# Kernel tuning notes

Measured on AMD Instinct MI355X. Metric: run time of the kernel, lower is better.

## Reference

```python
import jax, jax.numpy as jnp
import numpy as np

N, T, D, H, E, ED = 4096, 16, 5, 128, 32768, 32

def _leaky(x):
    return jnp.where(x >= 0, x, 0.2 * x)

def _lstm(x, Wih, Whh, bih, bhh):
    # x: [N, T, D] -> hidden sequence [N, T, H]; PyTorch gate order i,f,g,o
    pre = jnp.einsum('ntd,gd->tng', x, Wih) + bih + bhh  # [T, N, 4H]
    Hd = Whh.shape[1]
    def step(carry, p):
        h, c = carry
        g = p + h @ Whh.T
        i, f, gg, o = jnp.split(g, 4, axis=-1)
        c = jax.nn.sigmoid(f) * c + jax.nn.sigmoid(i) * jnp.tanh(gg)
        h = jax.nn.sigmoid(o) * jnp.tanh(c)
        return (h, c), h
    z = jnp.zeros((x.shape[0], Hd), x.dtype)
    _, hs = jax.lax.scan(step, (z, z), pre)
    return jnp.swapaxes(hs, 0, 1)

def _sire(x, src, dst, efeat, Wq, bq, Wk, bk, We, be, Wr, br):
    # SIREConv with agg_type='sum': m = LeakyReLU(eq[dst]+ek[src]+e); sum over in-edges; then linear_relation
    eq = x @ Wq.T + bq            # [N, T, H]
    ek = x @ Wk.T + bk            # [N, T, H]
    e = efeat @ We.T + be         # [E, H]
    m = _leaky(eq[dst] + ek[src] + e[:, None, :])  # [E, T, H]
    ft = jax.ops.segment_sum(m, dst, num_segments=x.shape[0])  # [N, T, H]
    return ft @ Wr.T + br

def _forward(stock_features, srcs, dsts, efeats, sire_ps, lstm_p, attn_p, mlp_p):
    sf = stock_features / jnp.mean(stock_features, axis=1, keepdims=True)
    sr = _lstm(sf, *lstm_p)  # [N, T, H]
    outs = [sr]
    for s, d, ef, p in zip(srcs, dsts, efeats, sire_ps):
        outs.append(_sire(sr, s, d, ef, *p))
    cat = jnp.concatenate(outs, axis=-1)  # [N, T, 4H]
    aw = jax.nn.softmax(cat @ attn_p[0].T + attn_p[1], axis=-2)  # softmax over time
    pooled = jnp.sum(cat * aw, axis=-2)   # [N, 4H]
    W1, b1, W2, b2 = mlp_p
    h = _leaky(pooled @ W1.T + b1)
    out = _leaky(h @ W2.T + b2)           # [N, 1]
    return out / sf[:, -1, 0:1] - 1.0


def setup_inputs() -> dict:
    key = jax.random.key(0)
    ks = iter(jax.random.split(key, 64))
    def nrm(shape, s=0.05):
        return jax.random.normal(next(ks), shape, jnp.float32) * s
    inp = {}
    inp['stock_features'] = jax.random.uniform(next(ks), (N, T, D), jnp.float32) + 0.5
    for g in ['wiki', 'industry', 'corr']:
        inp[g + '_src'] = jax.random.randint(next(ks), (E,), 0, N, jnp.int32)
        inp[g + '_dst'] = jax.random.randint(next(ks), (E,), 0, N, jnp.int32)
        inp[g + '_efeat'] = nrm((E, ED), 1.0)
        inp[g + '_Wq'] = nrm((H, H)); inp[g + '_bq'] = nrm((H,))
        inp[g + '_Wk'] = nrm((H, H)); inp[g + '_bk'] = nrm((H,))
        inp[g + '_We'] = nrm((H, ED)); inp[g + '_be'] = nrm((H,))
        inp[g + '_Wr'] = nrm((H, H)); inp[g + '_br'] = nrm((H,))
    inp['lstm_Wih'] = nrm((4 * H, D)); inp['lstm_Whh'] = nrm((4 * H, H))
    inp['lstm_bih'] = nrm((4 * H,)); inp['lstm_bhh'] = nrm((4 * H,))
    inp['attn_W'] = nrm((1, 4 * H)); inp['attn_b'] = nrm((1,))
    inp['mlp_W1'] = nrm((H, 4 * H)); inp['mlp_b1'] = nrm((H,))
    inp['mlp_W2'] = nrm((1, H)); inp['mlp_b2'] = nrm((1,))
    return inp


def reference(stock_features, wiki_src, wiki_dst, wiki_efeat,
              wiki_Wq, wiki_bq, wiki_Wk, wiki_bk, wiki_We, wiki_be, wiki_Wr, wiki_br,
              industry_src, industry_dst, industry_efeat,
              industry_Wq, industry_bq, industry_Wk, industry_bk, industry_We, industry_be, industry_Wr, industry_br,
              corr_src, corr_dst, corr_efeat,
              corr_Wq, corr_bq, corr_Wk, corr_bk, corr_We, corr_be, corr_Wr, corr_br,
              lstm_Wih, lstm_Whh, lstm_bih, lstm_bhh,
              attn_W, attn_b, mlp_W1, mlp_b1, mlp_W2, mlp_b2):
    srcs = (wiki_src, industry_src, corr_src)
    dsts = (wiki_dst, industry_dst, corr_dst)
    efeats = (wiki_efeat, industry_efeat, corr_efeat)
    sire_ps = ((wiki_Wq, wiki_bq, wiki_Wk, wiki_bk, wiki_We, wiki_be, wiki_Wr, wiki_br),
               (industry_Wq, industry_bq, industry_Wk, industry_bk, industry_We, industry_be, industry_Wr, industry_br),
               (corr_Wq, corr_bq, corr_Wk, corr_bk, corr_We, corr_be, corr_Wr, corr_br))
    return _forward(stock_features, srcs, dsts, efeats, sire_ps,
                    (lstm_Wih, lstm_Whh, lstm_bih, lstm_bhh),
                    (attn_W, attn_b), (mlp_W1, mlp_b1, mlp_W2, mlp_b2))
```

## Files before the change

### kernel.cpp

```cpp
#include <hip/hip_runtime.h>
#include <cstdint>
#include <cstddef>

#define NS 4096
#define TS 16
#define DF 5
#define HD 128
#define EE 32768
#define EDD 32

typedef __attribute__((ext_vector_type(8))) short bf16x8;
typedef __attribute__((ext_vector_type(4))) float f32x4;

__device__ __forceinline__ float sigmoidf_(float x){ return 1.f/(1.f+__expf(-x)); }
__device__ __forceinline__ float tanhf_(float x){ return 1.f - 2.f/(1.f+__expf(2.f*x)); }
__device__ __forceinline__ float leaky_(float x){ return x >= 0.f ? x : 0.2f*x; }

__device__ __forceinline__ unsigned short f2bf(float x){
  unsigned u = __float_as_uint(x);
  u += 0x7FFF + ((u>>16)&1);
  return (unsigned short)(u>>16);
}
__device__ __forceinline__ unsigned packbf(float a, float b){
  return (unsigned)f2bf(a) | ((unsigned)f2bf(b)<<16);
}
__device__ __forceinline__ void unpack2(unsigned u, float& a, float& b){
  a = __uint_as_float(u<<16);
  b = __uint_as_float(u & 0xFFFF0000u);
}
__device__ __forceinline__ void unpack8(uint4 q, float* f){
  unpack2(q.x, f[0], f[1]); unpack2(q.y, f[2], f[3]);
  unpack2(q.z, f[4], f[5]); unpack2(q.w, f[6], f[7]);
}
__device__ __forceinline__ bf16x8 ld_bf8(const unsigned short* p){
  union { uint4 u; bf16x8 v; } x; x.u = *(const uint4*)p; return x.v;
}

template<int ABF, int CBF>
__device__ __forceinline__ void gemm_dev(const void* Av, int lda,
    const float* __restrict__ Bp, int ldb, const float* __restrict__ bp,
    void* Cv, int ldc, int K, int act, size_t m0,
    unsigned short* Asb, unsigned short* Bsb)
{
  int tid = threadIdx.x;
  int wv = tid>>6, lane = tid&63, lm = lane&15, lq = lane>>4;
  f32x4 acc[2][8];
  #pragma unroll
  for (int mt=0;mt<2;mt++)
    #pragma unroll
    for (int nt=0;nt<8;nt++)
      acc[mt][nt] = (f32x4){0.f,0.f,0.f,0.f};

  for (int k0=0; k0<K; k0+=32){
    if (ABF){
      const unsigned short* A = (const unsigned short*)Av;
      #pragma unroll
      for (int rep=0;rep<2;rep++){
        int idx = tid + rep*256;
        int row = idx>>2, c8 = idx&3;
        *(uint4*)&Asb[row*40 + c8*8] = *(const uint4*)&A[(m0+row)*(size_t)lda + k0 + c8*8];
      }
    } else {
      const float* A = (const float*)Av;
      #pragma unroll
      for (int rep=0;rep<4;rep++){
        int idx = tid + rep*256;
        int row = idx>>3, c4 = idx&7;
        float4 a = *(const float4*)&A[(m0+row)*(size_t)lda + k0 + c4*4];
        *(uint2*)&Asb[row*40 + c4*4] = make_uint2(packbf(a.x,a.y), packbf(a.z,a.w));
      }
    }
    #pragma unroll
    for (int rep=0;rep<4;rep++){
      int idx = tid + rep*256;
      int row = idx>>3, c4 = idx&7;
      float4 b = *(const float4*)&Bp[(size_t)row*ldb + k0 + c4*4];
      *(uint2*)&Bsb[row*40 + c4*4] = make_uint2(packbf(b.x,b.y), packbf(b.z,b.w));
    }
    __syncthreads();
    bf16x8 afr[2], bfr[8];
    #pragma unroll
    for (int mt=0;mt<2;mt++)
      afr[mt] = ld_bf8(&Asb[(wv*32 + mt*16 + lm)*40 + lq*8]);
    #pragma unroll
    for (int nt=0;nt<8;nt++)
      bfr[nt] = ld_bf8(&Bsb[(nt*16 + lm)*40 + lq*8]);
    #pragma unroll
    for (int mt=0;mt<2;mt++)
      #pragma unroll
      for (int nt=0;nt<8;nt++)
        acc[mt][nt] = __builtin_amdgcn_mfma_f32_16x16x32_bf16(afr[mt], bfr[nt], acc[mt][nt], 0,0,0);
    __syncthreads();
  }

  #pragma unroll
  for (int mt=0;mt<2;mt++){
    #pragma unroll
    for (int nt=0;nt<8;nt++){
      int col = nt*16 + lm;
      float bv = bp[col];
      #pragma unroll
      for (int i=0;i<4;i++){
        float o = acc[mt][nt][i] + bv;
        if (act) o = leaky_(o);
        size_t ridx = (m0 + wv*32 + mt*16 + lq*4 + i)*(size_t)ldc + col;
        if (CBF) ((unsigned short*)Cv)[ridx] = f2bf(o);
        else     ((float*)Cv)[ridx] = o;
      }
    }
  }
}

__device__ void lstm8_dev(int blk, const float* __restrict__ sf,
                          const unsigned short* __restrict__ WhhB,
                          const float* __restrict__ Wih, const float* __restrict__ bih,
                          const float* __restrict__ bhh, unsigned short* __restrict__ cat,
                          char* smem)
{
  float* gates = (float*)smem;
  unsigned short* hbuf = (unsigned short*)(smem+16512);
  float* sfb = (float*)(smem+16512+2176);
  int tid = threadIdx.x;
  int n0 = blk*8;
  int wv = tid>>6, lane = tid&63, lm = lane&15, lq = lane>>4;

  bf16x8 bfr[8][4];
  #pragma unroll
  for (int nt=0;nt<8;nt++){
    int g = wv*128 + nt*16 + lm;
    #pragma unroll
    for (int kt=0;kt<4;kt++)
      bfr[nt][kt] = *(const bf16x8*)&WhhB[g*128 + kt*32 + lq*8];
  }

  int j = tid & 127;
  int rb = tid >> 7;
  float wih[4][5]; float bsum[4];
  #pragma unroll
  for (int gi=0; gi<4; gi++){
    int gc = gi*128 + j;
    #pragma unroll
    for (int d=0; d<5; d++) wih[gi][d] = Wih[gc*5+d];
    bsum[gi] = bih[gc] + bhh[gc];
  }
  float cst[4] = {0.f,0.f,0.f,0.f};

  for (int i=tid;i<544;i+=256) ((unsigned*)hbuf)[i] = 0;
  for (int i=tid;i<640;i+=256) sfb[i] = sf[(size_t)n0*80 + i];
  __syncthreads();

  bf16x8 zf = {0,0,0,0,0,0,0,0};
  for (int t=0;t<16;t++){
    bf16x8 af[4];
    #pragma unroll
    for (int kt=0;kt<4;kt++)
      af[kt] = (lm < 8) ? *(const bf16x8*)&hbuf[lm*136 + kt*32 + lq*8] : zf;
    #pragma unroll
    for (int nt=0;nt<8;nt++){
      f32x4 acc = {0.f,0.f,0.f,0.f};
      #pragma unroll
      for (int kt=0;kt<4;kt++)
        acc = __builtin_amdgcn_mfma_f32_16x16x32_bf16(af[kt], bfr[nt][kt], acc, 0,0,0);
      if (lq < 2){
        int col = wv*128 + nt*16 + lm;
        #pragma unroll
        for (int i=0;i<4;i++)
          gates[(lq*4+i)*516 + col] = acc[i];
      }
    }
    __syncthreads();
    #pragma unroll
    for (int q=0;q<4;q++){
      int r = rb + 2*q;
      const float* s = &sfb[r*80 + t*5];
      float pre[4];
      #pragma unroll
      for (int gi=0;gi<4;gi++){
        float a = bsum[gi];
        #pragma unroll
        for (int d=0;d<5;d++) a = fmaf(s[d], wih[gi][d], a);
        pre[gi] = a + gates[r*516 + gi*128 + j];
      }
      float iv = sigmoidf_(pre[0]);
      float fv = sigmoidf_(pre[1]);
      float gv = tanhf_(pre[2]);
      float ov = sigmoidf_(pre[3]);
      float c = fv*cst[q] + iv*gv;
      cst[q] = c;
      float h = ov*tanhf_(c);
      unsigned short hb16 = f2bf(h);
      hbuf[r*136 + j] = hb16;
      cat[(size_t)((n0+r)*16 + t)*512 + j] = hb16;
    }
    __syncthreads();
  }
}

__global__ __launch_bounds__(256)
void k_prolog(const float* __restrict__ x, float* __restrict__ sf,
              const float* __restrict__ Whh, unsigned short* __restrict__ whhB,
              int* __restrict__ cnt)
{
  int b = blockIdx.x, tid = threadIdx.x;
  if (b < 80){
    int id = b*256 + tid;
    if (id < NS*DF){
      int n = id / DF, d = id % DF;
      const float* xp = x + (size_t)n*TS*DF + d;
      float s = 0.f;
      #pragma unroll
      for (int t=0;t<TS;t++) s += xp[t*DF];
      float inv = (float)TS / s;
      float* sp = sf + (size_t)n*TS*DF + d;
      #pragma unroll
      for (int t=0;t<TS;t++) sp[t*DF] = xp[t*DF]*inv;
    }
  } else if (b < 336){
    int i = (b-80)*256 + tid;
    whhB[i] = f2bf(Whh[i]);
  } else {
    int i = (b-336)*256 + tid;
    cnt[i] = 0;
  }
}

struct M1 {
  const float *sf, *Wih, *bih, *bhh;
  const unsigned short* WhhB;
  unsigned short* cat;
  const float *ef[3]; const float *We[3]; const float *be[3];
  unsigned short* eeb;
  const int* dst[3];
  int* cnt;
};
__global__ __launch_bounds__(256,2)
void k_mega1(M1 p)
{
  __shared__ __align__(16) char smem[21504];
  int b = blockIdx.x;
  if (b < 512){
    lstm8_dev(b, p.sf, p.WhhB, p.Wih, p.bih, p.bhh, p.cat, smem);
  } else if (b < 1280){
    int idx = b - 512;
    int proj = idx % 3, mt = idx / 3;
    unsigned short* Asb = (unsigned short*)smem;
    unsigned short* Bsb = Asb + 128*40;
    gemm_dev<0,1>(p.ef[proj], 32, p.We[proj], 32, p.be[proj],
                  p.eeb + (size_t)proj*EE*128, 128, 32, 0, (size_t)mt*128, Asb, Bsb);
  } else {
    int idx = b - 1280;
    int g = idx >> 7, blk = idx & 127;
    int e = blk*256 + threadIdx.x;
    atomicAdd(&p.cnt[g*4096 + p.dst[g][e]], 1);
  }
}

__global__ __launch_bounds__(1024)
void k_scan(const int* __restrict__ cnt_, int* __restrict__ rs_, int* __restrict__ woff_){
  __shared__ int buf[1024];
  int g = blockIdx.x;
  const int* cnt = cnt_ + g*4096;
  int* rs = rs_ + g*4097;
  int* woff = woff_ + g*4096;
  int tid = threadIdx.x;
  int b = tid*4;
  int v0=cnt[b],v1=cnt[b+1],v2=cnt[b+2],v3=cnt[b+3];
  int s = v0+v1+v2+v3;
  buf[tid]=s;
  __syncthreads();
  for (int off=1; off<1024; off<<=1){
    int t = (tid>=off) ? buf[tid-off] : 0;
    __syncthreads();
    buf[tid] += t;
    __syncthreads();
  }
  int excl = buf[tid] - s;
  rs[b+0]=excl; woff[b+0]=excl; excl+=v0;
  rs[b+1]=excl; woff[b+1]=excl; excl+=v1;
  rs[b+2]=excl; woff[b+2]=excl; excl+=v2;
  rs[b+3]=excl; woff[b+3]=excl;
  if (tid==1023) rs[4096]=excl+v3;
}

struct M2 {
  const unsigned short* cat;
  const float* W[6]; const float* bias[6];
  unsigned short* eqk;
  const int* dst[3];
  int* woff; int* eidx;
};
__global__ __launch_bounds__(256)
void k_mega2(M2 p)
{
  __shared__ __align__(16) unsigned short Asb[128*40];
  __shared__ __align__(16) unsigned short Bsb[128*40];
  int b = blockIdx.x;
  if (b < 3072){
    int proj = b % 6, mt = b / 6;
    gemm_dev<1,1>(p.cat, 512, p.W[proj], 128, p.bias[proj],
                  p.eqk + (size_t)proj*NS*TS*128, 128, 128, 0, (size_t)mt*128, Asb, Bsb);
  } else {
    int idx = b - 3072;
    int g = idx >> 7, blk = idx & 127;
    int e = blk*256 + threadIdx.x;
    int pos = atomicAdd(&p.woff[g*4096 + p.dst[g][e]], 1);
    p.eidx[g*EE + pos] = e;
  }
}

struct P3 { const int* p[3]; };
__global__ __launch_bounds__(256)
void k_edge(const unsigned short* __restrict__ eqk, const unsigned short* __restrict__ eeb,
            P3 src, const int* __restrict__ rs_, const int* __restrict__ eidx_,
            unsigned short* __restrict__ ft_)
{
  int nb = blockIdx.x, t = blockIdx.y, g = blockIdx.z;
  const unsigned short* eqb = eqk + (size_t)(2*g)  *NS*TS*128;
  const unsigned short* ekb = eqk + (size_t)(2*g+1)*NS*TS*128;
  const unsigned short* eeg = eeb + (size_t)g*EE*128;
  unsigned short* ft = ft_ + (size_t)g*NS*TS*128;
  const int* srcp = src.p[g];
  const int* rs = rs_ + g*4097;
  const int* eidx = eidx_ + g*EE;
  int tid = threadIdx.x;
  int n = nb*16 + (tid>>4);
  int hb = (tid&15)*8;
  size_t own = ((size_t)(n*16+t))*128 + hb;
  float eqv[8], acc[8];
  unpack8(*(const uint4*)&eqb[own], eqv);
  #pragma unroll
  for (int j=0;j<8;j++) acc[j]=0.f;
  int i0 = rs[n], i1 = rs[n+1];
  for (int i=i0;i<i1;i++){
    int e = eidx[i];
    int s = srcp[e];
    uint4 kq = *(const uint4*)&ekb[((size_t)(s*16+t))*128 + hb];
    uint4 eq4 = *(const uint4*)&eeg[(size_t)e*128 + hb];
    float kf[8], ef[8];
    unpack8(kq, kf); unpack8(eq4, ef);
    #pragma unroll
    for (int j=0;j<8;j++)
      acc[j] += leaky_(eqv[j] + kf[j] + ef[j]);
  }
  uint4 o;
  o.x = packbf(acc[0],acc[1]); o.y = packbf(acc[2],acc[3]);
  o.z = packbf(acc[4],acc[5]); o.w = packbf(acc[6],acc[7]);
  *(uint4*)&ft[own] = o;
}

struct WrP {
  const unsigned short* A[3];
  const float* B[3]; const float* bias[3];
  unsigned short* C[3];
};
__global__ __launch_bounds__(256)
void k_wr(WrP p)
{
  __shared__ __align__(16) unsigned short Asb[128*40];
  __shared__ __align__(16) unsigned short Bsb[128*40];
  int proj = blockIdx.x;
  size_t m0 = (size_t)blockIdx.y * 128;
  gemm_dev<1,1>(p.A[proj], 128, p.B[proj], 128, p.bias[proj],
                p.C[proj], 512, 128, 0, m0, Asb, Bsb);
}

__global__ __launch_bounds__(256)
void k_attn(const unsigned short* __restrict__ cat, const float* __restrict__ attnW,
            const float* __restrict__ attnB, unsigned short* __restrict__ pooled)
{
  __shared__ unsigned short ct[16*512];
  __shared__ float sred[4][16];
  int n = blockIdx.x, tid = threadIdx.x;
  {
    const uint4* srcp = (const uint4*)(cat + (size_t)n*8192);
    uint4* dstp = (uint4*)ct;
    for (int i=tid;i<1024;i+=256) dstp[i] = srcp[i];
  }
  __syncthreads();
  int c0 = tid*2;
  float w0 = attnW[c0], w1 = attnW[c0+1];
  const unsigned* ctu = (const unsigned*)ct;
  float loc[16];
  #pragma unroll
  for (int t=0;t<16;t++){
    float a,b; unpack2(ctu[t*256 + tid], a, b);
    loc[t] = a*w0 + b*w1;
  }
  #pragma unroll
  for (int t=0;t<16;t++){
    float v = loc[t];
    for (int off=1; off<64; off<<=1) v += __shfl_xor(v, off, 64);
    loc[t]=v;
  }
  int wave = tid >> 6, lane = tid & 63;
  if (lane==0){
    #pragma unroll
    for (int t=0;t<16;t++) sred[wave][t]=loc[t];
  }
  __syncthreads();
  float s[16]; float m=-1e30f;
  float ab = attnB[0];
  #pragma unroll
  for (int t=0;t<16;t++){ s[t] = sred[0][t]+sred[1][t]+sred[2][t]+sred[3][t] + ab; m = fmaxf(m, s[t]); }
  float sum=0.f;
  #pragma unroll
  for (int t=0;t<16;t++){ s[t] = __expf(s[t]-m); sum += s[t]; }
  float inv = 1.f/sum;
  float p0=0.f,p1=0.f;
  #pragma unroll
  for (int t=0;t<16;t++){
    float a = s[t]*inv;
    float x,y; unpack2(ctu[t*256 + tid], x, y);
    p0 = fmaf(x, a, p0); p1 = fmaf(y, a, p1);
  }
  ((unsigned*)pooled)[(size_t)n*256 + tid] = packbf(p0,p1);
}

__global__ __launch_bounds__(256)
void k_mlp(const unsigned short* __restrict__ pooled, const float* __restrict__ W1,
           const float* __restrict__ b1, float* __restrict__ hmlp)
{
  __shared__ __align__(16) unsigned short Asb[128*40];
  __shared__ __align__(16) unsigned short Bsb[128*40];
  gemm_dev<1,0>(pooled, 512, W1, 512, b1, hmlp, 128, 512, 1,
                (size_t)blockIdx.x*128, Asb, Bsb);
}

__global__ __launch_bounds__(256)
void k_final(const float* __restrict__ hmlp, const float* __restrict__ W2,
             const float* __restrict__ b2, const float* __restrict__ sf,
             float* __restrict__ out)
{
  int tid = threadIdx.x;
  int n = blockIdx.x*4 + (tid>>6);
  int lane = tid & 63;
  const float* hp = hmlp + (size_t)n*128;
  float v = hp[lane]*W2[lane] + hp[64+lane]*W2[64+lane];
  for (int off=1; off<64; off<<=1) v += __shfl_xor(v, off, 64);
  if (lane==0){
    float o = v + b2[0];
    o = leaky_(o);
    out[n] = o / sf[(size_t)n*80 + 75] - 1.f;
  }
}

extern "C" void kernel_launch(void* const* d_in, const int* in_sizes, int n_in,
                              void* d_out, int out_size, void* d_ws, size_t ws_size,
                              hipStream_t stream)
{
  const float* x    = (const float*)d_in[0];
  const float* Wih  = (const float*)d_in[34];
  const float* Whh  = (const float*)d_in[35];
  const float* bih  = (const float*)d_in[36];
  const float* bhh  = (const float*)d_in[37];
  const float* attnW= (const float*)d_in[38];
  const float* attnB= (const float*)d_in[39];
  const float* W1   = (const float*)d_in[40];
  const float* b1   = (const float*)d_in[41];
  const float* W2   = (const float*)d_in[42];
  const float* b2   = (const float*)d_in[43];

  char* w = (char*)d_ws;
  size_t o = 0;
  unsigned short* cat    = (unsigned short*)(w+o); o += (size_t)NS*TS*512*2;
  unsigned short* eqk    = (unsigned short*)(w+o); o += (size_t)6*NS*TS*128*2;
  unsigned short* eeb    = (unsigned short*)(w+o); o += (size_t)3*EE*128*2;
  unsigned short* ft     = (unsigned short*)(w+o); o += (size_t)3*NS*TS*128*2;
  unsigned short* pooled = (unsigned short*)(w+o); o += (size_t)NS*512*2;
  float* sf   = (float*)(w+o); o += (size_t)NS*TS*DF*4;
  float* hmlp = (float*)(w+o); o += (size_t)NS*HD*4;
  unsigned short* whhB = (unsigned short*)(w+o); o += (size_t)512*128*2;
  int* cnt  = (int*)(w+o); o += 3*4096*4;
  int* rs   = (int*)(w+o); o += 3*4097*4;
  int* woff = (int*)(w+o); o += 3*4096*4;
  int* eidx = (int*)(w+o); o += (size_t)3*EE*4;

  P3 srcs = {{ (const int*)d_in[1], (const int*)d_in[12], (const int*)d_in[23] }};

  k_prolog<<<384, 256, 0, stream>>>(x, sf, Whh, whhB, cnt);

  {
    M1 p;
    p.sf = sf; p.Wih = Wih; p.bih = bih; p.bhh = bhh;
    p.WhhB = whhB; p.cat = cat; p.eeb = eeb; p.cnt = cnt;
    for (int g=0; g<3; g++){
      int base = 1 + g*11;
      p.ef[g] = (const float*)d_in[base+2];
      p.We[g] = (const float*)d_in[base+7];
      p.be[g] = (const float*)d_in[base+8];
      p.dst[g] = (const int*)d_in[base+1];
    }
    k_mega1<<<1664, 256, 0, stream>>>(p);
  }

  k_scan<<<3, 1024, 0, stream>>>(cnt, rs, woff);

  {
    M2 p;
    p.cat = cat; p.eqk = eqk; p.woff = woff; p.eidx = eidx;
    for (int g=0; g<3; g++){
      int base = 1 + g*11;
      p.W[2*g]      = (const float*)d_in[base+3];
      p.bias[2*g]   = (const float*)d_in[base+4];
      p.W[2*g+1]    = (const float*)d_in[base+5];
      p.bias[2*g+1] = (const float*)d_in[base+6];
      p.dst[g] = (const int*)d_in[base+1];
    }
    k_mega2<<<3456, 256, 0, stream>>>(p);
  }

  k_edge<<<dim3(256,16,3), 256, 0, stream>>>(eqk, eeb, srcs, rs, eidx, ft);

  {
    WrP p;
    for (int g=0; g<3; g++){
      int base = 1 + g*11;
      p.A[g]    = ft + (size_t)g*NS*TS*128;
      p.B[g]    = (const float*)d_in[base+9];
      p.bias[g] = (const float*)d_in[base+10];
      p.C[g]    = cat + (size_t)(1+g)*128;
    }
    k_wr<<<dim3(3,512), 256, 0, stream>>>(p);
  }

  k_attn<<<NS, 256, 0, stream>>>(cat, attnW, attnB, pooled);
  k_mlp<<<32, 256, 0, stream>>>(pooled, W1, b1, hmlp);
  k_final<<<NS/4, 256, 0, stream>>>(hmlp, W2, b2, sf, (float*)d_out);
}
```

Measured before the change: 416.0 us.

## Switch intermediates to fp16 with packed-half edge math and per-node edge blocks

Replaces the bf16 intermediate format with fp16 throughout: fp16 MFMA, hardware packed conversion (cvt_pkrtz) in place of manual bf16 rounding, and fp16 storage for cat, eqk, eeb, ft and pooled. The edge aggregation kernel now computes the leaky-ReLU on packed half vectors instead of unpacking to float, and the grid is remapped so one block handles all 16 timesteps of a single node. This cuts conversion ALU work and makes each node's CSR edge list and index loads shared across timesteps within a block. The cost is fp16 range and precision risk, and per-edge sums computed in half before float accumulation.

```diff
diff --git a/kernel.cpp b/kernel.cpp
--- a/kernel.cpp
+++ b/kernel.cpp
@@ -9,38 +9,33 @@
 #define EE 32768
 #define EDD 32
 
-typedef __attribute__((ext_vector_type(8))) short bf16x8;
+typedef _Float16 h16;
+typedef __attribute__((ext_vector_type(8))) _Float16 f16x8;
+typedef __attribute__((ext_vector_type(2))) __fp16 fp16x2_n;
 typedef __attribute__((ext_vector_type(4))) float f32x4;
 
 __device__ __forceinline__ float sigmoidf_(float x){ return 1.f/(1.f+__expf(-x)); }
 __device__ __forceinline__ float tanhf_(float x){ return 1.f - 2.f/(1.f+__expf(2.f*x)); }
 __device__ __forceinline__ float leaky_(float x){ return x >= 0.f ? x : 0.2f*x; }
 
-__device__ __forceinline__ unsigned short f2bf(float x){
-  unsigned u = __float_as_uint(x);
-  u += 0x7FFF + ((u>>16)&1);
-  return (unsigned short)(u>>16);
-}
-__device__ __forceinline__ unsigned packbf(float a, float b){
-  return (unsigned)f2bf(a) | ((unsigned)f2bf(b)<<16);
-}
-__device__ __forceinline__ void unpack2(unsigned u, float& a, float& b){
-  a = __uint_as_float(u<<16);
-  b = __uint_as_float(u & 0xFFFF0000u);
-}
-__device__ __forceinline__ void unpack8(uint4 q, float* f){
-  unpack2(q.x, f[0], f[1]); unpack2(q.y, f[2], f[3]);
-  unpack2(q.z, f[4], f[5]); unpack2(q.w, f[6], f[7]);
-}
-__device__ __forceinline__ bf16x8 ld_bf8(const unsigned short* p){
-  union { uint4 u; bf16x8 v; } x; x.u = *(const uint4*)p; return x.v;
-}
-
-template<int ABF, int CBF>
+__device__ __forceinline__ unsigned pkh(float a, float b){
+  union { fp16x2_n h; unsigned u; } x;
+  x.h = __builtin_amdgcn_cvt_pkrtz(a, b);
+  return x.u;
+}
+__device__ __forceinline__ void unpkh(unsigned u, float& a, float& b){
+  union { unsigned u; fp16x2_n h; } x; x.u = u;
+  a = (float)x.h.x; b = (float)x.h.y;
+}
+__device__ __forceinline__ f16x8 ld_h8(const h16* p){
+  union { uint4 u; f16x8 v; } x; x.u = *(const uint4*)p; return x.v;
+}
+
+template<int AH, int CH>
 __device__ __forceinline__ void gemm_dev(const void* Av, int lda,
     const float* __restrict__ Bp, int ldb, const float* __restrict__ bp,
     void* Cv, int ldc, int K, int act, size_t m0,
-    unsigned short* Asb, unsigned short* Bsb)
+    h16* Asb, h16* Bsb)
 {
   int tid = threadIdx.x;
   int wv = tid>>6, lane = tid&63, lm = lane&15, lq = lane>>4;
@@ -52,8 +47,8 @@
       acc[mt][nt] = (f32x4){0.f,0.f,0.f,0.f};
 
   for (int k0=0; k0<K; k0+=32){
-    if (ABF){
-      const unsigned short* A = (const unsigned short*)Av;
+    if (AH){
+      const h16* A = (const h16*)Av;
       #pragma unroll
       for (int rep=0;rep<2;rep++){
         int idx = tid + rep*256;
@@ -67,7 +62,7 @@
         int idx = tid + rep*256;
         int row = idx>>3, c4 = idx&7;
         float4 a = *(const float4*)&A[(m0+row)*(size_t)lda + k0 + c4*4];
-        *(uint2*)&Asb[row*40 + c4*4] = make_uint2(packbf(a.x,a.y), packbf(a.z,a.w));
+        *(uint2*)&Asb[row*40 + c4*4] = make_uint2(pkh(a.x,a.y), pkh(a.z,a.w));
       }
     }
     #pragma unroll
@@ -75,21 +70,21 @@
       int idx = tid + rep*256;
       int row = idx>>3, c4 = idx&7;
       float4 b = *(const float4*)&Bp[(size_t)row*ldb + k0 + c4*4];
-      *(uint2*)&Bsb[row*40 + c4*4] = make_uint2(packbf(b.x,b.y), packbf(b.z,b.w));
+      *(uint2*)&Bsb[row*40 + c4*4] = make_uint2(pkh(b.x,b.y), pkh(b.z,b.w));
     }
     __syncthreads();
-    bf16x8 afr[2], bfr[8];
+    f16x8 afr[2], bfr[8];
     #pragma unroll
     for (int mt=0;mt<2;mt++)
-      afr[mt] = ld_bf8(&Asb[(wv*32 + mt*16 + lm)*40 + lq*8]);
+      afr[mt] = ld_h8(&Asb[(wv*32 + mt*16 + lm)*40 + lq*8]);
     #pragma unroll
     for (int nt=0;nt<8;nt++)
-      bfr[nt] = ld_bf8(&Bsb[(nt*16 + lm)*40 + lq*8]);
+      bfr[nt] = ld_h8(&Bsb[(nt*16 + lm)*40 + lq*8]);
     #pragma unroll
     for (int mt=0;mt<2;mt++)
       #pragma unroll
       for (int nt=0;nt<8;nt++)
-        acc[mt][nt] = __builtin_amdgcn_mfma_f32_16x16x32_bf16(afr[mt], bfr[nt], acc[mt][nt], 0,0,0);
+        acc[mt][nt] = __builtin_amdgcn_mfma_f32_16x16x32_f16(afr[mt], bfr[nt], acc[mt][nt], 0,0,0);
     __syncthreads();
   }
 
@@ -104,33 +99,33 @@
         float o = acc[mt][nt][i] + bv;
         if (act) o = leaky_(o);
         size_t ridx = (m0 + wv*32 + mt*16 + lq*4 + i)*(size_t)ldc + col;
-        if (CBF) ((unsigned short*)Cv)[ridx] = f2bf(o);
-        else     ((float*)Cv)[ridx] = o;
+        if (CH) ((h16*)Cv)[ridx] = (h16)o;
+        else    ((float*)Cv)[ridx] = o;
       }
     }
   }
 }
 
 __device__ void lstm8_dev(int blk, const float* __restrict__ sf,
-                          const unsigned short* __restrict__ WhhB,
+                          const h16* __restrict__ WhhH,
                           const float* __restrict__ Wih, const float* __restrict__ bih,
-                          const float* __restrict__ bhh, unsigned short* __restrict__ cat,
+                          const float* __restrict__ bhh, h16* __restrict__ cat,
                           char* smem)
 {
   float* gates = (float*)smem;
-  unsigned short* hbuf = (unsigned short*)(smem+16512);
+  h16* hbuf = (h16*)(smem+16512);
   float* sfb = (float*)(smem+16512+2176);
   int tid = threadIdx.x;
   int n0 = blk*8;
   int wv = tid>>6, lane = tid&63, lm = lane&15, lq = lane>>4;
 
-  bf16x8 bfr[8][4];
+  f16x8 bfr[8][4];
   #pragma unroll
   for (int nt=0;nt<8;nt++){
     int g = wv*128 + nt*16 + lm;
     #pragma unroll
     for (int kt=0;kt<4;kt++)
-      bfr[nt][kt] = *(const bf16x8*)&WhhB[g*128 + kt*32 + lq*8];
+      bfr[nt][kt] = *(const f16x8*)&WhhH[g*128 + kt*32 + lq*8];
   }
 
   int j = tid & 127;
@@ -149,18 +144,18 @@
   for (int i=tid;i<640;i+=256) sfb[i] = sf[(size_t)n0*80 + i];
   __syncthreads();
 
-  bf16x8 zf = {0,0,0,0,0,0,0,0};
+  f16x8 zf = {0,0,0,0,0,0,0,0};
   for (int t=0;t<16;t++){
-    bf16x8 af[4];
+    f16x8 af[4];
     #pragma unroll
     for (int kt=0;kt<4;kt++)
-      af[kt] = (lm < 8) ? *(const bf16x8*)&hbuf[lm*136 + kt*32 + lq*8] : zf;
+      af[kt] = (lm < 8) ? *(const f16x8*)&hbuf[lm*136 + kt*32 + lq*8] : zf;
     #pragma unroll
     for (int nt=0;nt<8;nt++){
       f32x4 acc = {0.f,0.f,0.f,0.f};
       #pragma unroll
       for (int kt=0;kt<4;kt++)
-        acc = __builtin_amdgcn_mfma_f32_16x16x32_bf16(af[kt], bfr[nt][kt], acc, 0,0,0);
+        acc = __builtin_amdgcn_mfma_f32_16x16x32_f16(af[kt], bfr[nt][kt], acc, 0,0,0);
       if (lq < 2){
         int col = wv*128 + nt*16 + lm;
         #pragma unroll
@@ -188,9 +183,9 @@
       float c = fv*cst[q] + iv*gv;
       cst[q] = c;
       float h = ov*tanhf_(c);
-      unsigned short hb16 = f2bf(h);
-      hbuf[r*136 + j] = hb16;
-      cat[(size_t)((n0+r)*16 + t)*512 + j] = hb16;
+      h16 hh = (h16)h;
+      hbuf[r*136 + j] = hh;
+      cat[(size_t)((n0+r)*16 + t)*512 + j] = hh;
     }
     __syncthreads();
   }
@@ -198,7 +193,7 @@
 
 __global__ __launch_bounds__(256)
 void k_prolog(const float* __restrict__ x, float* __restrict__ sf,
-              const float* __restrict__ Whh, unsigned short* __restrict__ whhB,
+              const float* __restrict__ Whh, h16* __restrict__ whhH,
               int* __restrict__ cnt)
 {
   int b = blockIdx.x, tid = threadIdx.x;
@@ -217,7 +212,7 @@
     }
   } else if (b < 336){
     int i = (b-80)*256 + tid;
-    whhB[i] = f2bf(Whh[i]);
+    whhH[i] = (h16)Whh[i];
   } else {
     int i = (b-336)*256 + tid;
     cnt[i] = 0;
@@ -226,10 +221,10 @@
 
 struct M1 {
   const float *sf, *Wih, *bih, *bhh;
-  const unsigned short* WhhB;
-  unsigned short* cat;
+  const h16* WhhH;
+  h16* cat;
   const float *ef[3]; const float *We[3]; const float *be[3];
-  unsigned short* eeb;
+  h16* eeb;
   const int* dst[3];
   int* cnt;
 };
@@ -239,12 +234,12 @@
   __shared__ __align__(16) char smem[21504];
   int b = blockIdx.x;
   if (b < 512){
-    lstm8_dev(b, p.sf, p.WhhB, p.Wih, p.bih, p.bhh, p.cat, smem);
+    lstm8_dev(b, p.sf, p.WhhH, p.Wih, p.bih, p.bhh, p.cat, smem);
   } else if (b < 1280){
     int idx = b - 512;
     int proj = idx % 3, mt = idx / 3;
-    unsigned short* Asb = (unsigned short*)smem;
-    unsigned short* Bsb = Asb + 128*40;
+    h16* Asb = (h16*)smem;
+    h16* Bsb = Asb + 128*40;
     gemm_dev<0,1>(p.ef[proj], 32, p.We[proj], 32, p.be[proj],
                   p.eeb + (size_t)proj*EE*128, 128, 32, 0, (size_t)mt*128, Asb, Bsb);
   } else {
@@ -283,17 +278,17 @@
 }
 
 struct M2 {
-  const unsigned short* cat;
+  const h16* cat;
   const float* W[6]; const float* bias[6];
-  unsigned short* eqk;
+  h16* eqk;
   const int* dst[3];
   int* woff; int* eidx;
 };
 __global__ __launch_bounds__(256)
 void k_mega2(M2 p)
 {
-  __shared__ __align__(16) unsigned short Asb[128*40];
-  __shared__ __align__(16) unsigned short Bsb[128*40];
+  __shared__ __align__(16) h16 Asb[128*40];
+  __shared__ __align__(16) h16 Bsb[128*40];
   int b = blockIdx.x;
   if (b < 3072){
     int proj = b % 6, mt = b / 6;
@@ -310,54 +305,55 @@
 
 struct P3 { const int* p[3]; };
 __global__ __launch_bounds__(256)
-void k_edge(const unsigned short* __restrict__ eqk, const unsigned short* __restrict__ eeb,
+void k_edge(const h16* __restrict__ eqk, const h16* __restrict__ eeb,
             P3 src, const int* __restrict__ rs_, const int* __restrict__ eidx_,
-            unsigned short* __restrict__ ft_)
-{
-  int nb = blockIdx.x, t = blockIdx.y, g = blockIdx.z;
-  const unsigned short* eqb = eqk + (size_t)(2*g)  *NS*TS*128;
-  const unsigned short* ekb = eqk + (size_t)(2*g+1)*NS*TS*128;
-  const unsigned short* eeg = eeb + (size_t)g*EE*128;
-  unsigned short* ft = ft_ + (size_t)g*NS*TS*128;
+            h16* __restrict__ ft_)
+{
+  int n = blockIdx.x;
+  int g = blockIdx.y;
+  const h16* eqb = eqk + (size_t)(2*g)  *NS*TS*128;
+  const h16* ekb = eqk + (size_t)(2*g+1)*NS*TS*128;
+  const h16* eeg = eeb + (size_t)g*EE*128;
+  h16* ft = ft_ + (size_t)g*NS*TS*128;
   const int* srcp = src.p[g];
   const int* rs = rs_ + g*4097;
   const int* eidx = eidx_ + g*EE;
   int tid = threadIdx.x;
-  int n = nb*16 + (tid>>4);
-  int hb = (tid&15)*8;
+  int t = tid>>4, hb = (tid&15)*8;
   size_t own = ((size_t)(n*16+t))*128 + hb;
-  float eqv[8], acc[8];
-  unpack8(*(const uint4*)&eqb[own], eqv);
+  f16x8 eqv = ld_h8(&eqb[own]);
+  const f16x8 c02 = {(h16)0.2f,(h16)0.2f,(h16)0.2f,(h16)0.2f,
+                     (h16)0.2f,(h16)0.2f,(h16)0.2f,(h16)0.2f};
+  float acc[8];
   #pragma unroll
   for (int j=0;j<8;j++) acc[j]=0.f;
   int i0 = rs[n], i1 = rs[n+1];
   for (int i=i0;i<i1;i++){
     int e = eidx[i];
     int s = srcp[e];
-    uint4 kq = *(const uint4*)&ekb[((size_t)(s*16+t))*128 + hb];
-    uint4 eq4 = *(const uint4*)&eeg[(size_t)e*128 + hb];
-    float kf[8], ef[8];
-    unpack8(kq, kf); unpack8(eq4, ef);
-    #pragma unroll
-    for (int j=0;j<8;j++)
-      acc[j] += leaky_(eqv[j] + kf[j] + ef[j]);
+    f16x8 kv = ld_h8(&ekb[((size_t)(s*16+t))*128 + hb]);
+    f16x8 ev = ld_h8(&eeg[(size_t)e*128 + hb]);
+    f16x8 x = eqv + kv + ev;
+    f16x8 lk = __builtin_elementwise_max(x, x*c02);
+    #pragma unroll
+    for (int j=0;j<8;j++) acc[j] += (float)lk[j];
   }
   uint4 o;
-  o.x = packbf(acc[0],acc[1]); o.y = packbf(acc[2],acc[3]);
-  o.z = packbf(acc[4],acc[5]); o.w = packbf(acc[6],acc[7]);
+  o.x = pkh(acc[0],acc[1]); o.y = pkh(acc[2],acc[3]);
+  o.z = pkh(acc[4],acc[5]); o.w = pkh(acc[6],acc[7]);
   *(uint4*)&ft[own] = o;
 }
 
 struct WrP {
-  const unsigned short* A[3];
+  const h16* A[3];
   const float* B[3]; const float* bias[3];
-  unsigned short* C[3];
+  h16* C[3];
 };
 __global__ __launch_bounds__(256)
 void k_wr(WrP p)
 {
-  __shared__ __align__(16) unsigned short Asb[128*40];
-  __shared__ __align__(16) unsigned short Bsb[128*40];
+  __shared__ __align__(16) h16 Asb[128*40];
+  __shared__ __align__(16) h16 Bsb[128*40];
   int proj = blockIdx.x;
   size_t m0 = (size_t)blockIdx.y * 128;
   gemm_dev<1,1>(p.A[proj], 128, p.B[proj], 128, p.bias[proj],
@@ -365,10 +361,10 @@
 }
 
 __global__ __launch_bounds__(256)
-void k_attn(const unsigned short* __restrict__ cat, const float* __restrict__ attnW,
-            const float* __restrict__ attnB, unsigned short* __restrict__ pooled)
-{
-  __shared__ unsigned short ct[16*512];
+void k_attn(const h16* __restrict__ cat, const float* __restrict__ attnW,
+            const float* __restrict__ attnB, h16* __restrict__ pooled)
+{
+  __shared__ h16 ct[16*512];
   __shared__ float sred[4][16];
   int n = blockIdx.x, tid = threadIdx.x;
   {
@@ -383,7 +379,7 @@
   float loc[16];
   #pragma unroll
   for (int t=0;t<16;t++){
-    float a,b; unpack2(ctu[t*256 + tid], a, b);
+    float a,b; unpkh(ctu[t*256 + tid], a, b);
     loc[t] = a*w0 + b*w1;
   }
   #pragma unroll
@@ -410,18 +406,18 @@
   #pragma unroll
   for (int t=0;t<16;t++){
     float a = s[t]*inv;
-    float x,y; unpack2(ctu[t*256 + tid], x, y);
+    float x,y; unpkh(ctu[t*256 + tid], x, y);
     p0 = fmaf(x, a, p0); p1 = fmaf(y, a, p1);
   }
-  ((unsigned*)pooled)[(size_t)n*256 + tid] = packbf(p0,p1);
-}
-
-__global__ __launch_bounds__(256)
-void k_mlp(const unsigned short* __restrict__ pooled, const float* __restrict__ W1,
+  ((unsigned*)pooled)[(size_t)n*256 + tid] = pkh(p0,p1);
+}
+
+__global__ __launch_bounds__(256)
+void k_mlp(const h16* __restrict__ pooled, const float* __restrict__ W1,
            const float* __restrict__ b1, float* __restrict__ hmlp)
 {
-  __shared__ __align__(16) unsigned short Asb[128*40];
-  __shared__ __align__(16) unsigned short Bsb[128*40];
+  __shared__ __align__(16) h16 Asb[128*40];
+  __shared__ __align__(16) h16 Bsb[128*40];
   gemm_dev<1,0>(pooled, 512, W1, 512, b1, hmlp, 128, 512, 1,
                 (size_t)blockIdx.x*128, Asb, Bsb);
 }
@@ -462,14 +458,14 @@
 
   char* w = (char*)d_ws;
   size_t o = 0;
-  unsigned short* cat    = (unsigned short*)(w+o); o += (size_t)NS*TS*512*2;
-  unsigned short* eqk    = (unsigned short*)(w+o); o += (size_t)6*NS*TS*128*2;
-  unsigned short* eeb    = (unsigned short*)(w+o); o += (size_t)3*EE*128*2;
-  unsigned short* ft     = (unsigned short*)(w+o); o += (size_t)3*NS*TS*128*2;
-  unsigned short* pooled = (unsigned short*)(w+o); o += (size_t)NS*512*2;
+  h16* cat    = (h16*)(w+o); o += (size_t)NS*TS*512*2;
+  h16* eqk    = (h16*)(w+o); o += (size_t)6*NS*TS*128*2;
+  h16* eeb    = (h16*)(w+o); o += (size_t)3*EE*128*2;
+  h16* ft     = (h16*)(w+o); o += (size_t)3*NS*TS*128*2;
+  h16* pooled = (h16*)(w+o); o += (size_t)NS*512*2;
   float* sf   = (float*)(w+o); o += (size_t)NS*TS*DF*4;
   float* hmlp = (float*)(w+o); o += (size_t)NS*HD*4;
-  unsigned short* whhB = (unsigned short*)(w+o); o += (size_t)512*128*2;
+  h16* whhH = (h16*)(w+o); o += (size_t)512*128*2;
   int* cnt  = (int*)(w+o); o += 3*4096*4;
   int* rs   = (int*)(w+o); o += 3*4097*4;
   int* woff = (int*)(w+o); o += 3*4096*4;
@@ -477,12 +473,12 @@
 
   P3 srcs = {{ (const int*)d_in[1], (const int*)d_in[12], (const int*)d_in[23] }};
 
-  k_prolog<<<384, 256, 0, stream>>>(x, sf, Whh, whhB, cnt);
+  k_prolog<<<384, 256, 0, stream>>>(x, sf, Whh, whhH, cnt);
 
   {
     M1 p;
     p.sf = sf; p.Wih = Wih; p.bih = bih; p.bhh = bhh;
-    p.WhhB = whhB; p.cat = cat; p.eeb = eeb; p.cnt = cnt;
+    p.WhhH = whhH; p.cat = cat; p.eeb = eeb; p.cnt = cnt;
     for (int g=0; g<3; g++){
       int base = 1 + g*11;
       p.ef[g] = (const float*)d_in[base+2];
@@ -509,7 +505,7 @@
     k_mega2<<<3456, 256, 0, stream>>>(p);
   }
 
-  k_edge<<<dim3(256,16,3), 256, 0, stream>>>(eqk, eeb, srcs, rs, eidx, ft);
+  k_edge<<<dim3(NS,3), 256, 0, stream>>>(eqk, eeb, srcs, rs, eidx, ft);
 
   {
     WrP p;
```

After: 380.4 us. -8.6%, faster.
